# Optimization experiments

Hardware: AMD Instinct MI355X
Metric: run time of the kernel (lower is better)

The kernel has to match this reference:

```python
import jax, jax.numpy as jnp
import numpy as np

# dataset config constants
FOV_UP = 3.0 / 180.0 * np.pi
FOV_DOWN = -25.0 / 180.0 * np.pi
FOV_RANGE = abs(FOV_DOWN) + abs(FOV_UP)
DEPTH_SCALE = 6.0
DEPTH_MIN, DEPTH_MAX = 1.0, 63.0
LOG_SCALE = True
H, W = 64, 2048
B = 64


def _trig_buffers():
    scan_x = np.arange(W, dtype=np.float64) / W          # (W,)
    scan_y = np.arange(H, dtype=np.float64) / H          # (H,)
    yaw = np.pi * (scan_x * 2.0 - 1.0)                   # (W,)
    pitch = (1.0 - scan_y) * FOV_RANGE - abs(FOV_DOWN)   # (H,)
    yaw2d = np.broadcast_to(yaw[None, :], (H, W))
    pitch2d = np.broadcast_to(pitch[:, None], (H, W))
    f32 = lambda a: jnp.asarray(a, dtype=jnp.float32)
    return (f32(np.cos(yaw2d)), f32(np.sin(yaw2d)),
            f32(np.cos(pitch2d)), f32(np.sin(pitch2d)))


def setup_inputs() -> dict:
    key = jax.random.key(0)
    x = jax.random.normal(key, (B, 1, H, W), dtype=jnp.float32)
    return {"x": x}


def _range2xyz(imgs):
    cos_yaw, sin_yaw, cos_pitch, sin_pitch = _trig_buffers()
    depth = (imgs * 0.5 + 0.5) * DEPTH_SCALE              # (B,1,H,W)
    if LOG_SCALE:
        depth = jnp.exp2(depth) - 1.0
    depth = jnp.clip(depth, DEPTH_MIN, DEPTH_MAX)
    bx = cos_yaw * cos_pitch * depth
    by = -sin_yaw * cos_pitch * depth
    bz = sin_pitch * depth
    return jnp.concatenate([bx, by, bz], axis=1)          # (B,3,H,W)


def _curvature(xyz):
    # 1x11 depthwise conv along W, kernel [1]*5 + [-10] + [1]*5, pad 5
    k = jnp.array([1, 1, 1, 1, 1, -10, 1, 1, 1, 1, 1], dtype=jnp.float32)
    rhs = jnp.tile(k.reshape(1, 1, 1, 11), (3, 1, 1, 1))  # (O=3, I/g=1, 1, 11)
    d = jax.lax.conv_general_dilated(
        xyz, rhs, window_strides=(1, 1), padding=[(0, 0), (5, 5)],
        dimension_numbers=("NCHW", "OIHW", "NCHW"), feature_group_count=3)
    cloud_curvature = jnp.sum(d * d, axis=1, keepdims=True)   # (B,1,H,W)

    depth = jnp.sqrt(jnp.sum(xyz * xyz, axis=1))              # (B,H,W)
    dxyz = xyz[:, :, :, 1:] - xyz[:, :, :, :-1]               # (B,3,H,W-1)
    diff = jnp.sqrt(jnp.sum(dxyz * dxyz, axis=1))             # (B,H,W-1)
    zpad = jnp.zeros((B, H, 1), dtype=xyz.dtype)
    diff = jnp.concatenate([diff, zpad], axis=-1)             # (B,H,W)
    mask1 = diff > 0.1

    depth_ratio = depth[:, :, 1:] / depth[:, :, :-1]          # (B,H,W-1)
    dr = xyz[:, :, :, 1:] - xyz[:, :, :, :-1] * depth_ratio[:, None]
    diff_ratio = jnp.sqrt(jnp.sum(dr * dr, axis=1))           # (B,H,W-1)
    opad = jnp.ones((B, H, 1), dtype=xyz.dtype)
    diff_ratio = jnp.concatenate([opad, diff_ratio], axis=-1)
    mask2 = diff_ratio < 0.1

    picked = jnp.zeros((B, H, W), dtype=bool)
    picked = picked.at[:, :, 5:-6].set(mask1[:, :, 5:-6] & mask2[:, :, 5:-6])

    # diff2 in the original is mathematically identical to diff (squared diffs)
    diff2 = diff
    dis = jnp.sum(xyz * xyz, axis=1)                          # (B,H,W)
    outlier = (diff > 0.0002 * dis) & (diff2 > 0.0002 * dis)
    picked = picked | outlier

    inf = jnp.asarray(jnp.inf, dtype=cloud_curvature.dtype)
    return jnp.where(picked[:, None, :, :], inf, cloud_curvature)


def reference(x):
    x = x / 2.0 + 0.5
    xyz = _range2xyz(x)
    return _curvature(xyz)
```

## Files before the change

### kernel.cpp

```cpp
#include <hip/hip_runtime.h>
#include <math.h>

#define WW 2048
#define HH 64
#define NROW 4096

#define PICKED_F_BITS 0x7F7F0000u

typedef float f32x4 __attribute__((ext_vector_type(4)));
typedef float f32x2 __attribute__((ext_vector_type(2)));
typedef unsigned int u32x4 __attribute__((ext_vector_type(4)));

static __device__ inline int adr(int sc) { return sc + (sc >> 3); }

__global__ __launch_bounds__(256) void curv_kernel(
    const float* __restrict__ x, unsigned short* __restrict__ out) {
  __shared__ float sd[2324];

  const int t   = threadIdx.x;
  const int row = blockIdx.x;
  const int h   = row & (HH - 1);
  const size_t base = (size_t)row * WW;
  const int c0  = 8 * t;

  f32x4 x0 = *(const f32x4*)(x + base + c0);
  f32x4 x1 = *(const f32x4*)(x + base + c0 + 4);

  const float inv2pi = 0.15915494309189535f;
  const float prad =
      (1.0f - (float)h * (1.0f / 64.0f)) * 0.48869219055841229f
      - 0.43633231299858238f;
  const float cp  = __builtin_amdgcn_cosf(prad * inv2pi);
  const float sp  = __builtin_amdgcn_sinf(prad * inv2pi);
  const float sp2 = sp * sp;
  const float cp2 = cp * cp;

  const float C1    = 4.706190423e-6f;
  const float gamma = 2.0f - 2.0f * C1 * cp2;
  const float Q     = 1062.4329f * __builtin_amdgcn_rcpf(cp2);

  const float CDU[18] = {
      0.99988234745421256f, 0.99992470183914450f, 0.99995764455196390f,
      0.99998117528260111f, 0.99999529380957619f, 1.0f,
      0.99999529380957619f, 0.99998117528260111f, 0.99995764455196390f,
      0.99992470183914450f, 0.99988234745421256f, 0.99983058179582340f,
      0.99976940535121528f, 0.99969881869620425f, 0.99961882249517864f,
      0.99952941750109314f, 0.99943060455546173f, 0.99932238458834954f};
  const float SDU[18] = {
      -0.015339206284988102f, -0.012271538285719925f, -0.0092037547820598194f,
      -0.0061358846491544753f, -0.0030679567629659763f, 0.0f,
      0.0030679567629659763f, 0.0061358846491544753f, 0.0092037547820598194f,
      0.012271538285719925f, 0.015339206284988102f, 0.018406729905804820f,
      0.021474080275469508f, 0.024541228522912288f, 0.027608145778965740f,
      0.030674803176636626f, 0.033741171851377587f, 0.036807222941358832f};

  float wd[18];

  #pragma unroll
  for (int e = 0; e < 8; ++e) {
    const float v = (e < 4) ? x0[e] : x1[e - 4];
    const float arg = __builtin_amdgcn_fmed3f(v * 1.5f + 4.5f, 1.0f, 6.0f);
    const float dpt = __builtin_amdgcn_exp2f(arg) - 1.0f;
    wd[5 + e] = dpt;
    sd[adr(c0 + 8 + e)] = dpt;
  }
  if (t < 8) sd[adr(t)] = 0.0f;
  else if (t >= 248) sd[adr(t + 1808)] = 0.0f;
  __syncthreads();

  #pragma unroll
  for (int i = 0; i < 5; ++i) {
    wd[i]      = sd[adr(c0 + 3 + i)];
    wd[13 + i] = sd[adr(c0 + 16 + i)];
  }

  float Sx = 0.f, Sy = 0.f, Sw = 0.f;
  #pragma unroll
  for (int u = 0; u <= 10; ++u) {
    Sx = fmaf(wd[u], CDU[u], Sx);
    Sy = fmaf(wd[u], SDU[u], Sy);
    Sw += wd[u];
  }

  const bool tn0 = (t != 0), tn255 = (t != 255);
  u32x4 ov;

  #pragma unroll
  for (int p = 0; p < 4; ++p) {
    const int j0 = 2 * p, j1 = 2 * p + 1;
    if (p > 0) {
      const float eW = wd[j0 + 10], lW = wd[j0 - 1];
      Sx = fmaf(eW, CDU[j0 + 10], fmaf(lW, -CDU[j0 - 1], Sx));
      Sy = fmaf(eW, SDU[j0 + 10], fmaf(lW, -SDU[j0 - 1], Sy));
      Sw += eW - lW;
    }
    const float S0x = Sx, S0y = Sy, S0w = Sw;
    {
      const float eW = wd[j1 + 10], lW = wd[j1 - 1];
      Sx = fmaf(eW, CDU[j1 + 10], fmaf(lW, -CDU[j1 - 1], Sx));
      Sy = fmaf(eW, SDU[j1 + 10], fmaf(lW, -SDU[j1 - 1], Sy));
      Sw += eW - lW;
    }

    const f32x2 VSx = {S0x, Sx}, VSy = {S0y, Sy}, VSw = {S0w, Sw};
    const f32x2 cd  = {wd[j0 + 5], wd[j1 + 5]};
    const f32x2 nd  = {wd[j0 + 6], wd[j1 + 6]};
    const f32x2 nCc = {-11.0f * CDU[j0 + 5], -11.0f * CDU[j1 + 5]};
    const f32x2 nCs = {-11.0f * SDU[j0 + 5], -11.0f * SDU[j1 + 5]};

    const f32x2 dxv = cd * nCc + VSx;
    const f32x2 dyv = cd * nCs + VSy;
    const f32x2 tdz = cd * -11.0f + VSw;
    const f32x2 curv = (dxv * dxv + dyv * dyv) * cp2 + (tdz * tdz) * sp2;

    const f32x2 dis_c = cd * cd;
    const f32x2 dis_n = nd * nd;
    const f32x2 m     = cd * nd;
    f32x2 d2 = (dis_c + dis_n) - m * gamma;
    if (p == 3) d2.y = tn255 ? d2.y : 0.0f;
    const f32x2 sv = dis_c * 2.0e-4f;
    const f32x2 s2 = sv * sv;

    const bool wok0 = (j0 < 2) ? tn0 : ((j0 < 5) ? (tn0 && tn255) : tn255);
    const bool wok1 = (j1 < 2) ? tn0 : ((j1 < 5) ? (tn0 && tn255) : tn255);
    const bool p0 =
        ((d2.x > 0.01f) && (dis_c.x < Q) && wok0) || (d2.x > s2.x);
    const bool p1 =
        ((d2.y > 0.01f) && (dis_c.y < Q) && wok1) || (d2.y > s2.y);
    const float r0 = p0 ? __builtin_bit_cast(float, PICKED_F_BITS) : curv.x;
    const float r1 = p1 ? __builtin_bit_cast(float, PICKED_F_BITS) : curv.y;

    ov[p] = __builtin_amdgcn_perm(
        __builtin_bit_cast(unsigned int, r1),
        __builtin_bit_cast(unsigned int, r0), 0x07060302u);
  }
  *(u32x4*)(out + base + c0) = ov;
}

extern "C" void kernel_launch(void* const* d_in, const int* in_sizes, int n_in,
                              void* d_out, int out_size, void* d_ws, size_t ws_size,
                              hipStream_t stream) {
  const float* x = (const float*)d_in[0];
  unsigned short* out = (unsigned short*)d_out;
  (void)d_ws; (void)ws_size; (void)in_sizes; (void)n_in; (void)out_size;
  curv_kernel<<<NROW, 256, 0, stream>>>(x, out);
}
```

Measured before the change: 14.41 us.

## Process 16 columns per thread and two rows per block

Each thread now handles 16 consecutive columns instead of 8, and each 256-thread block covers two image rows with separate shared-memory halves, halving the block count. The sliding-window sums are reused across more outputs, which reduces the per-output share of halo loads from shared memory and of per-row trig and constant setup. The shared-memory padding scheme changes to three pad words every 16 to suit the new access stride. In exchange, each thread uses more registers (26-entry window plus two output vectors), there is less parallelism per row, and the per-thread global loads and stores become wider and fewer.

```diff
diff --git a/kernel.cpp b/kernel.cpp
--- a/kernel.cpp
+++ b/kernel.cpp
@@ -3,7 +3,7 @@
 
 #define WW 2048
 #define HH 64
-#define NROW 4096
+#define NBLK 2048
 
 #define PICKED_F_BITS 0x7F7F0000u
 
@@ -11,20 +11,24 @@
 typedef float f32x2 __attribute__((ext_vector_type(2)));
 typedef unsigned int u32x4 __attribute__((ext_vector_type(4)));
 
-static __device__ inline int adr(int sc) { return sc + (sc >> 3); }
+static __device__ inline int adr(int sc) { return sc + 3 * (sc >> 4); }
 
 __global__ __launch_bounds__(256) void curv_kernel(
     const float* __restrict__ x, unsigned short* __restrict__ out) {
-  __shared__ float sd[2324];
+  __shared__ float sd[2][2448];
 
   const int t   = threadIdx.x;
-  const int row = blockIdx.x;
+  const int tt  = t & 127;
+  const int rr  = t >> 7;
+  const int row = 2 * blockIdx.x + rr;
   const int h   = row & (HH - 1);
   const size_t base = (size_t)row * WW;
-  const int c0  = 8 * t;
+  const int c0  = 16 * tt;
+  float* sdr = sd[rr];
 
-  f32x4 x0 = *(const f32x4*)(x + base + c0);
-  f32x4 x1 = *(const f32x4*)(x + base + c0 + 4);
+  f32x4 xq[4];
+  #pragma unroll
+  for (int q = 0; q < 4; ++q) xq[q] = *(const f32x4*)(x + base + c0 + 4 * q);
 
   const float inv2pi = 0.15915494309189535f;
   const float prad =
@@ -39,39 +43,43 @@
   const float gamma = 2.0f - 2.0f * C1 * cp2;
   const float Q     = 1062.4329f * __builtin_amdgcn_rcpf(cp2);
 
-  const float CDU[18] = {
+  const float CDU[26] = {
       0.99988234745421256f, 0.99992470183914450f, 0.99995764455196390f,
       0.99998117528260111f, 0.99999529380957619f, 1.0f,
       0.99999529380957619f, 0.99998117528260111f, 0.99995764455196390f,
       0.99992470183914450f, 0.99988234745421256f, 0.99983058179582340f,
       0.99976940535121528f, 0.99969881869620425f, 0.99961882249517864f,
-      0.99952941750109314f, 0.99943060455546173f, 0.99932238458834954f};
-  const float SDU[18] = {
+      0.99952941750109314f, 0.99943060455546173f, 0.99932238458834954f,
+      0.99920475858f, 0.99907772773f, 0.99894129311f, 0.99879545620f,
+      0.99864021818f, 0.99847558058f, 0.99830154703f, 0.99811811290f};
+  const float SDU[26] = {
       -0.015339206284988102f, -0.012271538285719925f, -0.0092037547820598194f,
       -0.0061358846491544753f, -0.0030679567629659763f, 0.0f,
       0.0030679567629659763f, 0.0061358846491544753f, 0.0092037547820598194f,
       0.012271538285719925f, 0.015339206284988102f, 0.018406729905804820f,
       0.021474080275469508f, 0.024541228522912288f, 0.027608145778965740f,
-      0.030674803176636626f, 0.033741171851377587f, 0.036807222941358832f};
+      0.030674803176636626f, 0.033741171851377587f, 0.036807222941358832f,
+      0.0398729276f, 0.0429382560f, 0.0460031822f, 0.0490676743f,
+      0.0521317030f, 0.0551952410f, 0.0582582600f, 0.0613207240f};
 
-  float wd[18];
+  float wd[26];
 
   #pragma unroll
-  for (int e = 0; e < 8; ++e) {
-    const float v = (e < 4) ? x0[e] : x1[e - 4];
+  for (int e = 0; e < 16; ++e) {
+    const float v = xq[e >> 2][e & 3];
     const float arg = __builtin_amdgcn_fmed3f(v * 1.5f + 4.5f, 1.0f, 6.0f);
     const float dpt = __builtin_amdgcn_exp2f(arg) - 1.0f;
     wd[5 + e] = dpt;
-    sd[adr(c0 + 8 + e)] = dpt;
+    sdr[adr(c0 + 8 + e)] = dpt;
   }
-  if (t < 8) sd[adr(t)] = 0.0f;
-  else if (t >= 248) sd[adr(t + 1808)] = 0.0f;
+  if (tt < 8) sdr[adr(tt)] = 0.0f;
+  else if (tt >= 120) sdr[adr(tt + 1936)] = 0.0f;
   __syncthreads();
 
   #pragma unroll
   for (int i = 0; i < 5; ++i) {
-    wd[i]      = sd[adr(c0 + 3 + i)];
-    wd[13 + i] = sd[adr(c0 + 16 + i)];
+    wd[i]      = sdr[adr(c0 + 3 + i)];
+    wd[21 + i] = sdr[adr(c0 + 24 + i)];
   }
 
   float Sx = 0.f, Sy = 0.f, Sw = 0.f;
@@ -82,11 +90,12 @@
     Sw += wd[u];
   }
 
-  const bool tn0 = (t != 0), tn255 = (t != 255);
-  u32x4 ov;
+  const bool tn0 = (tt != 0), tn127 = (tt != 127);
+  const float pickedf = __builtin_bit_cast(float, PICKED_F_BITS);
+  u32x4 ov0, ov1;
 
   #pragma unroll
-  for (int p = 0; p < 4; ++p) {
+  for (int p = 0; p < 8; ++p) {
     const int j0 = 2 * p, j1 = 2 * p + 1;
     if (p > 0) {
       const float eW = wd[j0 + 10], lW = wd[j0 - 1];
@@ -117,24 +126,26 @@
     const f32x2 dis_n = nd * nd;
     const f32x2 m     = cd * nd;
     f32x2 d2 = (dis_c + dis_n) - m * gamma;
-    if (p == 3) d2.y = tn255 ? d2.y : 0.0f;
+    if (p == 7) d2.y = tn127 ? d2.y : 0.0f;
     const f32x2 sv = dis_c * 2.0e-4f;
     const f32x2 s2 = sv * sv;
 
-    const bool wok0 = (j0 < 2) ? tn0 : ((j0 < 5) ? (tn0 && tn255) : tn255);
-    const bool wok1 = (j1 < 2) ? tn0 : ((j1 < 5) ? (tn0 && tn255) : tn255);
+    const bool wok0 = (j0 < 5 ? tn0 : true) && (j0 > 9 ? tn127 : true);
+    const bool wok1 = (j1 < 5 ? tn0 : true) && (j1 > 9 ? tn127 : true);
     const bool p0 =
         ((d2.x > 0.01f) && (dis_c.x < Q) && wok0) || (d2.x > s2.x);
     const bool p1 =
         ((d2.y > 0.01f) && (dis_c.y < Q) && wok1) || (d2.y > s2.y);
-    const float r0 = p0 ? __builtin_bit_cast(float, PICKED_F_BITS) : curv.x;
-    const float r1 = p1 ? __builtin_bit_cast(float, PICKED_F_BITS) : curv.y;
+    const float r0 = p0 ? pickedf : curv.x;
+    const float r1 = p1 ? pickedf : curv.y;
 
-    ov[p] = __builtin_amdgcn_perm(
+    const unsigned int pk = __builtin_amdgcn_perm(
         __builtin_bit_cast(unsigned int, r1),
         __builtin_bit_cast(unsigned int, r0), 0x07060302u);
+    if (p < 4) ov0[p] = pk; else ov1[p - 4] = pk;
   }
-  *(u32x4*)(out + base + c0) = ov;
+  *(u32x4*)(out + base + c0) = ov0;
+  *(u32x4*)(out + base + c0 + 8) = ov1;
 }
 
 extern "C" void kernel_launch(void* const* d_in, const int* in_sizes, int n_in,
@@ -143,5 +154,5 @@
   const float* x = (const float*)d_in[0];
   unsigned short* out = (unsigned short*)d_out;
   (void)d_ws; (void)ws_size; (void)in_sizes; (void)n_in; (void)out_size;
-  curv_kernel<<<NROW, 256, 0, stream>>>(x, out);
+  curv_kernel<<<NBLK, 256, 0, stream>>>(x, out);
 }
```

Measured after the change: 15.33 us. +6.4%, slower.
